# Performance work log

Hardware: AMD Instinct MI355X
Metric: run time of the kernel (lower is better)

Reference implementation:

```python
import jax, jax.numpy as jnp
import numpy as np

LOSS_WEIGHT = 1.0
BIG = 1e9  # finite sentinel for masked-out pixels (avoids inf-grad NaNs)


def setup_inputs() -> dict:
    key = jax.random.key(0)
    k1, k2 = jax.random.split(key)
    B, N, H, W = 4, 6890, 64, 64
    vert2d = jax.random.uniform(k1, (B, N, 2), dtype=jnp.float32) * jnp.array([W, H], jnp.float32)
    mask = jax.random.randint(k2, (B, H, W), 0, 2, dtype=jnp.int32)
    return {"vert2d": vert2d, "mask": mask}


def reference(vert2d, mask):
    B, N, _ = vert2d.shape
    _, H, W = mask.shape
    scale = jnp.array([W, H], vert2d.dtype)
    v = vert2d / scale  # [B,N,2], normalized
    # all pixel coords as (x, y), normalized -- the dense equivalent of torch.where points
    ys, xs = jnp.meshgrid(jnp.arange(H), jnp.arange(W), indexing="ij")
    pts = (jnp.stack([xs.ravel(), ys.ravel()], axis=-1).astype(v.dtype) / scale)  # [HW,2]
    valid = (mask.reshape(B, -1) > 0)  # [B,HW] boolean membership of each pixel
    # pairwise L2 distances: [B,N,HW]
    diff = v[:, :, None, :] - pts[None, None, :, :]
    d = jnp.sqrt(jnp.sum(diff * diff, axis=-1))
    dm = jnp.where(valid[:, None, :], d, BIG)
    # sum over mask points of min over verts  +  sum over verts of min over mask points
    loss = jnp.sum(jnp.min(dm, axis=1) * valid) + jnp.sum(jnp.min(dm, axis=2))
    return LOSS_WEIGHT * loss
```

## Files before the change

### kernel.cpp

```cpp
#include <hip/hip_runtime.h>

#define NB 4
#define NV 6890
#define HW 4096
#define NPAD 6912
#define T1CS 108
#define T1_BLOCKS 512
#define T2_BLOCKS 512
#define NELEM 44032
#define NRED_BLOCKS 16

#define OFF_T1  0
#define OFF_T2  65536

#define FINF 3.402823466e38f
#define VBIG 1.0e9f
#define PBIG 1.0e18f

__global__ __launch_bounds__(256) void k_main(const float* __restrict__ vert,
                                              const int* __restrict__ mask,
                                              unsigned* __restrict__ t1,
                                              unsigned* __restrict__ t2) {
    __shared__ float4 lds4[64];
    float2* lds2 = reinterpret_cast<float2*>(lds4);
    int bx = blockIdx.x, tid = threadIdx.x;
    if (bx < T1_BLOCKS) {
        int c = bx & 63, q = (bx >> 6) & 1, b = bx >> 7;
        if (tid < T1CS) {
            int n = c * T1CS + tid;
            float2 w = make_float2(VBIG, 0.f);
            if (n < NV) w = reinterpret_cast<const float2*>(vert)[b * NV + n];
            lds2[tid] = w;
        }
        __syncthreads();
        int x = tid & 63, ry = tid >> 6;
        float fx = (float)x;
        float fm2x = -2.f * fx, fx2 = fx * fx;
        float fm2y[8], m[8];
        #pragma unroll
        for (int k = 0; k < 8; ++k) {
            fm2y[k] = -2.f * (float)(q * 32 + ry + 4 * k);
            m[k] = FINF;
        }
        #pragma unroll 6
        for (int i = 0; i < T1CS / 2; ++i) {
            float4 a = lds4[i];
            float vva = fmaf(a.x, a.x, a.y * a.y);
            float vvb = fmaf(a.z, a.z, a.w * a.w);
            float ta  = fmaf(fm2x, a.x, vva);
            float tb  = fmaf(fm2x, a.z, vvb);
            #pragma unroll
            for (int k = 0; k < 8; ++k) {
                float da = fmaf(fm2y[k], a.y, ta);
                float db = fmaf(fm2y[k], a.w, tb);
                m[k] = fminf(m[k], fminf(da, db));
            }
        }
        unsigned* tp = t1 + (b << 12) + x;
        #pragma unroll
        for (int k = 0; k < 8; ++k) {
            int y = q * 32 + ry + 4 * k;
            float fy = (float)y;
            float mf = fmaxf(fmaf(fy, fy, fx2) + m[k], 0.f);
            atomicMin(tp + y * 64, __float_as_uint(mf));
        }
    } else {
        int t2i = bx - T1_BLOCKS;
        int y = t2i & 63, rest = t2i >> 6;
        int g = rest & 1, b = rest >> 1;
        if (tid < 64) {
            int pix = y * 64 + tid;
            float fx = (float)tid;
            float e = (mask[b * HW + pix] > 0) ? fx * fx : PBIG;
            lds2[tid] = make_float2(-2.f * fx, e);
        }
        __syncthreads();
        int n0 = g * 4096 + tid;
        const float2* vv2 = reinterpret_cast<const float2*>(vert) + b * NV;
        float fy = (float)y, fm2y = -2.f * fy;
        float vx[16], base[16], mr[16];
        bool val[16];
        #pragma unroll
        for (int k = 0; k < 16; ++k) {
            int n = n0 + 256 * k;
            val[k] = (n < NV);
            float2 t = val[k] ? vv2[n] : make_float2(0.f, 0.f);
            vx[k] = t.x;
            float vv = fmaf(t.x, t.x, t.y * t.y);
            base[k] = fmaf(fm2y, t.y, fmaf(fy, fy, vv));
            mr[k] = FINF;
        }
        #pragma unroll 4
        for (int j = 0; j < 32; ++j) {
            float4 a = lds4[j];
            #pragma unroll
            for (int k = 0; k < 16; ++k) {
                float da = fmaf(a.x, vx[k], a.y);
                float db = fmaf(a.z, vx[k], a.w);
                mr[k] = fminf(mr[k], fminf(da, db));
            }
        }
        unsigned* op = t2 + b * NPAD + n0;
        #pragma unroll
        for (int k = 0; k < 16; ++k)
            if (val[k]) {
                float mf = fmaxf(mr[k] + base[k], 0.f);
                atomicMin(op + 256 * k, __float_as_uint(mf));
            }
    }
}

__global__ __launch_bounds__(256) void k_red(const unsigned* __restrict__ t1,
                                             const unsigned* __restrict__ t2,
                                             const int* __restrict__ mask,
                                             float* __restrict__ out) {
    int tid = threadIdx.x;
    float v = 0.f;
    for (int gid = blockIdx.x * 256 + tid; gid < NELEM; gid += NRED_BLOCKS * 256) {
        float e = 0.f;
        if (gid < NB * HW) {
            if (mask[gid] > 0)
                e = sqrtf(fmaxf(__uint_as_float(t1[gid]), 0.f));
        } else {
            int j = gid - NB * HW;
            int b = j / NPAD;
            int n = j - b * NPAD;
            if (n < NV)
                e = sqrtf(fmaxf(__uint_as_float(t2[j]), 0.f));
        }
        v += e;
    }
    v *= (1.0f / 64.0f);
    __shared__ float sbuf[4];
    for (int off = 32; off; off >>= 1) v += __shfl_down(v, off, 64);
    int lane = tid & 63, wid = tid >> 6;
    if (!lane) sbuf[wid] = v;
    __syncthreads();
    if (tid == 0)
        atomicAdd(out, sbuf[0] + sbuf[1] + sbuf[2] + sbuf[3]);
}

extern "C" void kernel_launch(void* const* d_in, const int* in_sizes, int n_in,
                              void* d_out, int out_size, void* d_ws, size_t ws_size,
                              hipStream_t stream) {
    const float* vert = (const float*)d_in[0];
    const int*   mask = (const int*)d_in[1];
    char* ws = (char*)d_ws;
    unsigned* t1  = (unsigned*)(ws + OFF_T1);
    unsigned* t2  = (unsigned*)(ws + OFF_T2);
    float*    out = (float*)d_out;

    k_main<<<T1_BLOCKS + T2_BLOCKS, 256, 0, stream>>>(vert, mask, t1, t2);
    k_red <<<NRED_BLOCKS, 256, 0, stream>>>(t1, t2, mask, out);
}
```

Measured before the change: 74.30 us.

## Fuse final reduction into main kernel via last-block ticket counter

```diff
diff --git a/kernel.cpp b/kernel.cpp
--- a/kernel.cpp
+++ b/kernel.cpp
@@ -7,23 +7,30 @@
 #define T1CS 108
 #define T1_BLOCKS 512
 #define T2_BLOCKS 512
+#define NBLK 1024
 #define NELEM 44032
-#define NRED_BLOCKS 16
+#define POISON 0xAAAAAAAAu
 
 #define OFF_T1  0
 #define OFF_T2  65536
+#define OFF_TKT 176128
 
 #define FINF 3.402823466e38f
 #define VBIG 1.0e9f
 #define PBIG 1.0e18f
 
-__global__ __launch_bounds__(256) void k_main(const float* __restrict__ vert,
-                                              const int* __restrict__ mask,
-                                              unsigned* __restrict__ t1,
-                                              unsigned* __restrict__ t2) {
+__global__ __launch_bounds__(256) void k_all(const float* __restrict__ vert,
+                                             const int* __restrict__ mask,
+                                             unsigned* __restrict__ t1,
+                                             unsigned* __restrict__ t2,
+                                             unsigned* __restrict__ tkt,
+                                             float* __restrict__ out) {
     __shared__ float4 lds4[64];
+    __shared__ unsigned my_s;
+    __shared__ float sbuf[4];
     float2* lds2 = reinterpret_cast<float2*>(lds4);
     int bx = blockIdx.x, tid = threadIdx.x;
+
     if (bx < T1_BLOCKS) {
         int c = bx & 63, q = (bx >> 6) & 1, b = bx >> 7;
         if (tid < T1CS) {
@@ -108,36 +115,38 @@
                 atomicMin(op + 256 * k, __float_as_uint(mf));
             }
     }
-}
 
-__global__ __launch_bounds__(256) void k_red(const unsigned* __restrict__ t1,
-                                             const unsigned* __restrict__ t2,
-                                             const int* __restrict__ mask,
-                                             float* __restrict__ out) {
-    int tid = threadIdx.x;
+    __syncthreads();
+    if (tid == 0) my_s = atomicAdd(tkt, 1u);
+    __syncthreads();
+    if (my_s != POISON + (NBLK - 1)) return;
+
     float v = 0.f;
-    for (int gid = blockIdx.x * 256 + tid; gid < NELEM; gid += NRED_BLOCKS * 256) {
+    for (int gid = tid; gid < NELEM; gid += 256) {
         float e = 0.f;
         if (gid < NB * HW) {
-            if (mask[gid] > 0)
-                e = sqrtf(fmaxf(__uint_as_float(t1[gid]), 0.f));
+            if (mask[gid] > 0) {
+                unsigned raw = atomicMin(&t1[gid], 0xFFFFFFFFu);
+                e = sqrtf(fmaxf(__uint_as_float(raw), 0.f));
+            }
         } else {
             int j = gid - NB * HW;
             int b = j / NPAD;
             int n = j - b * NPAD;
-            if (n < NV)
-                e = sqrtf(fmaxf(__uint_as_float(t2[j]), 0.f));
+            if (n < NV) {
+                unsigned raw = atomicMin(&t2[j], 0xFFFFFFFFu);
+                e = sqrtf(fmaxf(__uint_as_float(raw), 0.f));
+            }
         }
         v += e;
     }
     v *= (1.0f / 64.0f);
-    __shared__ float sbuf[4];
     for (int off = 32; off; off >>= 1) v += __shfl_down(v, off, 64);
     int lane = tid & 63, wid = tid >> 6;
     if (!lane) sbuf[wid] = v;
     __syncthreads();
     if (tid == 0)
-        atomicAdd(out, sbuf[0] + sbuf[1] + sbuf[2] + sbuf[3]);
+        out[0] = sbuf[0] + sbuf[1] + sbuf[2] + sbuf[3];
 }
 
 extern "C" void kernel_launch(void* const* d_in, const int* in_sizes, int n_in,
@@ -148,8 +157,8 @@
     char* ws = (char*)d_ws;
     unsigned* t1  = (unsigned*)(ws + OFF_T1);
     unsigned* t2  = (unsigned*)(ws + OFF_T2);
+    unsigned* tkt = (unsigned*)(ws + OFF_TKT);
     float*    out = (float*)d_out;
 
-    k_main<<<T1_BLOCKS + T2_BLOCKS, 256, 0, stream>>>(vert, mask, t1, t2);
-    k_red <<<NRED_BLOCKS, 256, 0, stream>>>(t1, t2, mask, out);
+    k_all<<<NBLK, 256, 0, stream>>>(vert, mask, t1, t2, tkt, out);
 }
```

New measurement: 152.9 us. +105.8%, slower.
